# Kernel tuning notes

Hardware: AMD Instinct MI355X
Metric: run time of the kernel (lower is better)

## Reference

```python
import jax, jax.numpy as jnp
import numpy as np

N_LEVELS = 16; BASE = 16; SCALE = 2.0; L2HASH = 19; LEVEL_DIM = 2; BOUND = 2.0
RES = [int(np.ceil(BASE * SCALE ** i)) for i in range(N_LEVELS)]
# level-0 table size; the torch source uses embeddings[0].num_embeddings as the
# modulus for ALL levels (kept faithful). T0 = min(16^3, 2^19) = 4096.
T0 = min(RES[0] ** 3, 2 ** L2HASH)
# 4096 is a power of two, so hash % 4096 only depends on low 12 bits -> reduce
# primes mod T0 and work in int32 (matches torch's int64 math exactly).
PRIMES = (np.array([1, 2654435761, 805459861], dtype=np.int64) % T0).astype(np.int32)
# corner order matches the torch triple loop: dx outer, dy, dz inner
OFFS = np.array([[dx, dy, dz] for dx in (0, 1) for dy in (0, 1) for dz in (0, 1)], dtype=np.int32)


def _hash(c):
    # c: int32 [..., 3], already clamped to [0, res-1]
    return ((c[..., 0] * PRIMES[0]) ^ (c[..., 1] * PRIMES[1]) ^ (c[..., 2] * PRIMES[2])) % T0


def _hash_encode(pn, emb):
    # pn: [N,3] normalized positions; emb: [L, T0, 2]
    outs = []
    for li, res in enumerate(RES):
        scaled = (pn + 1.0) * 0.5 * (res - 1)            # [N,3]
        gc = jnp.floor(scaled).astype(jnp.int32)
        w = scaled - gc.astype(scaled.dtype)             # trilinear weights [N,3]
        corners = jnp.clip(gc[:, None, :] + OFFS[None], 0, res - 1)  # [N,8,3]
        f = emb[li][_hash(corners)]                      # gather -> [N,8,2]
        wx, wy, wz = w[:, 0:1], w[:, 1:2], w[:, 2:3]
        c00 = f[:, 0] * (1 - wx) + f[:, 1] * wx
        c01 = f[:, 2] * (1 - wx) + f[:, 3] * wx
        c10 = f[:, 4] * (1 - wx) + f[:, 5] * wx
        c11 = f[:, 6] * (1 - wx) + f[:, 7] * wx
        c0 = c00 * (1 - wy) + c01 * wy
        c1 = c10 * (1 - wy) + c11 * wy
        outs.append(c0 * (1 - wz) + c1 * wz)
    return jnp.concatenate(outs, -1)                     # [N, 32]


def _sh16(d):
    n = jnp.maximum(jnp.linalg.norm(d, axis=-1, keepdims=True), 1e-12)
    d = d / n
    x, y, z = d[..., 0], d[..., 1], d[..., 2]
    feats = [
        0.28209479177387814 * jnp.ones_like(x),
        -0.48860251190291987 * y, 0.48860251190291987 * z, -0.48860251190291987 * x,
        1.0925484305920792 * x * y, -1.0925484305920792 * y * z,
        0.31539156525252005 * (2 * z ** 2 - x ** 2 - y ** 2),
        -1.0925484305920792 * x * z, 0.5462742152960396 * (x ** 2 - y ** 2),
        -0.5900435899266435 * y * (3 * x ** 2 - y ** 2), 2.890611442640554 * x * y * z,
        -0.4570457994644658 * y * (4 * z ** 2 - x ** 2 - y ** 2),
        0.3731763325901154 * z * (2 * z ** 2 - 3 * x ** 2 - 3 * y ** 2),
        -0.4570457994644658 * x * (4 * z ** 2 - x ** 2 - y ** 2),
        1.445305721320277 * z * (x ** 2 - y ** 2),
        -0.5900435899266435 * x * (x ** 2 - 3 * y ** 2),
    ]
    return jnp.stack(feats, -1)                          # [N, 16]


def setup_inputs() -> dict:
    key = jax.random.key(0)
    ks = jax.random.split(key, 20)
    N = 1_000_000
    def lin(k, i, o):
        return jax.random.normal(k, (i, o), jnp.float32) * (1.0 / np.sqrt(i))
    return {
        'positions': jax.random.uniform(ks[0], (N, 3), jnp.float32),  # in [0,1) c [-bound,bound]
        'directions': jax.random.normal(ks[1], (N, 3), jnp.float32),
        'emb': jax.random.uniform(ks[2], (N_LEVELS, T0, LEVEL_DIM), jnp.float32, -1e-4, 1e-4),
        'gw0': lin(ks[3], 32, 64), 'gb0': jnp.zeros((64,), jnp.float32),
        'gw1': lin(ks[4], 64, 64), 'gb1': jnp.zeros((64,), jnp.float32),
        'dw': lin(ks[5], 64, 16), 'db': jnp.zeros((16,), jnp.float32),
        'cw0': lin(ks[6], 31, 64), 'cb0': jnp.zeros((64,), jnp.float32),
        'cw1': lin(ks[7], 64, 64), 'cb1': jnp.zeros((64,), jnp.float32),
        'cw2': lin(ks[8], 64, 64), 'cb2': jnp.zeros((64,), jnp.float32),
        'rw': lin(ks[9], 64, 3), 'rb': jnp.zeros((3,), jnp.float32),
    }


def reference(positions, directions, emb, gw0, gb0, gw1, gb1, dw, db,
              cw0, cb0, cw1, cb1, cw2, cb2, rw, rb):
    pn = positions / BOUND
    enc = _hash_encode(pn, emb)                          # [N,32]
    h = jax.nn.relu(enc @ gw0 + gb0)
    h = jax.nn.relu(h @ gw1 + gb1)
    g = h @ dw + db                                      # [N, 1+15]
    density = jnp.exp(g[:, 0:1] - 1.0)                   # exp activation, bias -1.0
    geo_feat = g[:, 1:]
    c = jnp.concatenate([geo_feat, _sh16(directions)], -1)  # [N,31]
    c = jax.nn.relu(c @ cw0 + cb0)
    c = c @ cw1 + cb1                                    # NOTE: no ReLU (faithful to source)
    c = c @ cw2 + cb2
    rgb = jax.nn.sigmoid(c @ rw + rb)
    return density, rgb
```

## Files before the change

kernel.cpp:

```cpp
#include <hip/hip_runtime.h>
#include <hip/hip_bf16.h>
#include <math.h>

#define BLK 256
#define TT  4096
#define WSETS 36

typedef short bf16x8 __attribute__((ext_vector_type(8)));
typedef float f32x4  __attribute__((ext_vector_type(4)));

__device__ __forceinline__ unsigned pk(float a, float b) {
  __hip_bfloat162 h = __float22bfloat162_rn(make_float2(a, b));
  unsigned r; __builtin_memcpy(&r, &h, sizeof(r));
  return r;
}
__device__ __forceinline__ bf16x8 mk8(unsigned w0, unsigned w1, unsigned w2, unsigned w3) {
  uint4 u; u.x = w0; u.y = w1; u.z = w2; u.w = w3;
  bf16x8 r; __builtin_memcpy(&r, &u, 16);
  return r;
}
__device__ __forceinline__ bf16x8 ld8(const uint4* __restrict__ wsW, int set, int lane) {
  uint4 u = wsW[set * 64 + lane];
  bf16x8 r; __builtin_memcpy(&r, &u, 16);
  return r;
}
__device__ __forceinline__ float bflo(unsigned w) {
  return __builtin_bit_cast(float, w << 16);
}
__device__ __forceinline__ float bfhi(unsigned w) {
  return __builtin_bit_cast(float, w & 0xFFFF0000u);
}
__device__ __forceinline__ f32x4 mfma16(bf16x8 a, bf16x8 b, f32x4 c) {
  return __builtin_amdgcn_mfma_f32_16x16x32_bf16(a, b, c, 0, 0, 0);
}

__global__ void ngp_pack(const float* __restrict__ emb,
                         const float* __restrict__ gw0, const float* __restrict__ gw1,
                         const float* __restrict__ dw,  const float* __restrict__ cw0,
                         const float* __restrict__ cw1, const float* __restrict__ cw2,
                         const float* __restrict__ rw,  unsigned* __restrict__ ws)
{
  int i = blockIdx.x * blockDim.x + threadIdx.x;
  if (i < 16 * TT) {
    const float* s = emb + 2 * (size_t)i;
    ws[i] = pk(s[0], s[1]);
    return;
  }
  i -= 16 * TT;
  if (i >= WSETS * 64) return;
  int s = i >> 6, l = i & 63;
  int q = l >> 4, p = l & 15;

  const float* W; int out = 64, mt = 0, kt = 0, typ = 0;
  if      (s < 4)  { W = gw0; mt = s; }
  else if (s < 12) { W = gw1; mt = (s - 4) >> 1;  kt = (s - 4) & 1; }
  else if (s < 14) { W = dw;  out = 16; kt = s - 12; }
  else if (s < 18) { W = cw0; mt = s - 14; typ = 1; }
  else if (s < 26) { W = cw1; mt = (s - 18) >> 1; kt = (s - 18) & 1; }
  else if (s < 34) { W = cw2; mt = (s - 26) >> 1; kt = (s - 26) & 1; }
  else             { W = rw;  out = 3; kt = s - 34; typ = 2; }
  int f = (out == 16) ? p : ((out == 3) ? p : mt * 16 + p);
  float v[8];
  #pragma unroll
  for (int j = 0; j < 8; ++j) {
    int k = kt * 32 + q * 8 + j;
    if (typ == 1)      v[j] = (k == 0) ? 0.0f : W[(k - 1) * 64 + f];
    else if (typ == 2) v[j] = (p < 3) ? W[k * 3 + p] : 0.0f;
    else               v[j] = W[k * out + f];
  }
  uint4 wv;
  wv.x = pk(v[0], v[1]); wv.y = pk(v[2], v[3]);
  wv.z = pk(v[4], v[5]); wv.w = pk(v[6], v[7]);
  ((uint4*)(ws + 16 * TT))[s * 64 + l] = wv;
}

__device__ __forceinline__ bf16x8 bfrag_pt(const unsigned (&ep)[16], int src, int q) {
  bf16x8 b;
  #pragma unroll
  for (int w = 0; w < 4; ++w) {
    int v0 = __shfl((int)ep[w],      src);
    int v1 = __shfl((int)ep[4 + w],  src);
    int v2 = __shfl((int)ep[8 + w],  src);
    int v3 = __shfl((int)ep[12 + w], src);
    int lo = (q & 1) ? v1 : v0;
    int hi = (q & 1) ? v3 : v2;
    unsigned word = (unsigned)((q & 2) ? hi : lo);
    b[2 * w]     = (short)(word & 0xFFFFu);
    b[2 * w + 1] = (short)(word >> 16);
  }
  return b;
}

template<int KT_>
__device__ __forceinline__ bf16x8 bfrag_u(const unsigned (&unt)[4][2], int q, int p) {
  bf16x8 b;
  #pragma unroll
  for (int w = 0; w < 4; ++w) {
    int src = (((2 * q + (w >> 1)) & 3) << 4) + p;
    int v0 = __shfl((int)unt[2 * KT_][w & 1],     src);
    int v1 = __shfl((int)unt[2 * KT_ + 1][w & 1], src);
    unsigned word = (unsigned)((q >> 1) ? v1 : v0);
    b[2 * w]     = (short)(word & 0xFFFFu);
    b[2 * w + 1] = (short)(word >> 16);
  }
  return b;
}

__device__ __forceinline__ bf16x8 bfrag_cat(const unsigned (&g2nt)[2], const unsigned (&shp)[8],
                                            int srcP, int q, int p) {
  bf16x8 b;
  #pragma unroll
  for (int w = 0; w < 4; ++w) {
    int srcG = (((2 * q + (w >> 1)) & 3) << 4) + p;
    int vg = __shfl((int)g2nt[w & 1], srcG);
    int v2 = __shfl((int)shp[w],      srcP);
    int v3 = __shfl((int)shp[4 + w],  srcP);
    unsigned word = (q < 2) ? (unsigned)vg : ((q == 2) ? (unsigned)v2 : (unsigned)v3);
    b[2 * w]     = (short)(word & 0xFFFFu);
    b[2 * w + 1] = (short)(word >> 16);
  }
  return b;
}

template<bool PRE, bool RELU>
__device__ __forceinline__ void layer64(const float* __restrict__ W, const uint4* __restrict__ wsW,
                                        int base, const float* __restrict__ bias,
                                        const unsigned (&uin)[4][4][2], unsigned (&uout)[4][4][2],
                                        int lane, int q, int p) {
  bf16x8 A[4][2];
  #pragma unroll
  for (int mt = 0; mt < 4; ++mt)
    #pragma unroll
    for (int kt = 0; kt < 2; ++kt) {
      if (PRE) {
        A[mt][kt] = ld8(wsW, base + mt * 2 + kt, lane);
      } else {
        const float* Wb = W + (kt * 32 + 8 * q) * 64 + mt * 16 + p;
        A[mt][kt] = mk8(pk(Wb[0 * 64], Wb[1 * 64]), pk(Wb[2 * 64], Wb[3 * 64]),
                        pk(Wb[4 * 64], Wb[5 * 64]), pk(Wb[6 * 64], Wb[7 * 64]));
      }
    }
  f32x4 bi[4];
  #pragma unroll
  for (int mt = 0; mt < 4; ++mt) bi[mt] = *(const f32x4*)(bias + mt * 16 + 4 * q);
  #pragma unroll
  for (int nt = 0; nt < 4; ++nt) {
    bf16x8 B0 = bfrag_u<0>(uin[nt], q, p);
    bf16x8 B1 = bfrag_u<1>(uin[nt], q, p);
    #pragma unroll
    for (int mt = 0; mt < 4; ++mt) {
      f32x4 acc = bi[mt];
      acc = mfma16(A[mt][0], B0, acc);
      acc = mfma16(A[mt][1], B1, acc);
      if (RELU) {
        acc.x = fmaxf(acc.x, 0.0f); acc.y = fmaxf(acc.y, 0.0f);
        acc.z = fmaxf(acc.z, 0.0f); acc.w = fmaxf(acc.w, 0.0f);
      }
      uout[nt][mt][0] = pk(acc.x, acc.y);
      uout[nt][mt][1] = pk(acc.z, acc.w);
    }
  }
}

template<bool PRE>
__global__ __launch_bounds__(BLK, 4)
void ngp_fused9(const float* __restrict__ pos,  const float* __restrict__ dirs,
                const float* __restrict__ emb,  const unsigned* __restrict__ wsTab,
                const float* __restrict__ gw0, const float* __restrict__ gb0,
                const float* __restrict__ gw1, const float* __restrict__ gb1,
                const float* __restrict__ dw,  const float* __restrict__ db,
                const float* __restrict__ cw0, const float* __restrict__ cb0,
                const float* __restrict__ cw1, const float* __restrict__ cb1,
                const float* __restrict__ cw2, const float* __restrict__ cb2,
                const float* __restrict__ rw,  const float* __restrict__ rb,
                float* __restrict__ outd, float* __restrict__ outrgb, int N)
{
  __shared__ unsigned tab[2][TT];

  const int tid  = threadIdx.x;
  const int lane = tid & 63, wave = tid >> 6;
  const int q = lane >> 4, p = lane & 15;
  const int idx = blockIdx.x * BLK + tid;
  const int ic = min(idx, N - 1);
  const int ptb = blockIdx.x * BLK + wave * 64;
  const uint4* wsW = (const uint4*)(wsTab + 16 * TT);

  const float pnx = pos[3 * ic + 0] * 0.5f;
  const float pny = pos[3 * ic + 1] * 0.5f;
  const float pnz = pos[3 * ic + 2] * 0.5f;

  auto stage = [&](int li) {
    if (PRE) {
      const uint4* s4 = (const uint4*)(wsTab + (size_t)li * TT);
      uint4* dst = (uint4*)tab[li & 1];
      #pragma unroll
      for (int j = 0; j < (TT / 4) / BLK; ++j)
        dst[tid + j * BLK] = s4[tid + j * BLK];
    } else {
      const f32x4* s4 = (const f32x4*)(emb + (size_t)li * (TT * 2));
      uint2* dst = (uint2*)tab[li & 1];
      #pragma unroll
      for (int j = 0; j < (TT / 2) / BLK; ++j) {
        f32x4 v = s4[tid + j * BLK];
        uint2 w; w.x = pk(v.x, v.y); w.y = pk(v.z, v.w);
        dst[tid + j * BLK] = w;
      }
    }
  };

  float enc[32];
  stage(0);
  __syncthreads();
  #pragma unroll
  for (int li = 0; li < 16; ++li) {
    if (li < 15) stage(li + 1);
    const unsigned* t = tab[li & 1];
    const int   res = 16 << li;
    const float rm1 = (float)(res - 1);
    float sx = (pnx + 1.0f) * 0.5f * rm1;
    float sy = (pny + 1.0f) * 0.5f * rm1;
    float sz = (pnz + 1.0f) * 0.5f * rm1;
    float fx = floorf(sx), fy = floorf(sy), fz = floorf(sz);
    float wx = sx - fx,    wy = sy - fy,    wz = sz - fz;
    int ix = (int)fx, iy = (int)fy, iz = (int)fz;
    int x0 = min(max(ix, 0),     res - 1), x1 = min(max(ix + 1, 0), res - 1);
    int y0 = min(max(iy, 0),     res - 1), y1 = min(max(iy + 1, 0), res - 1);
    int z0 = min(max(iz, 0),     res - 1), z1 = min(max(iz + 1, 0), res - 1);
    unsigned a0 = (unsigned)x0,         a1 = (unsigned)x1;
    unsigned b0 = (unsigned)y0 * 2481u, b1 = (unsigned)y1 * 2481u;
    unsigned d0 = (unsigned)z0 * 1941u, d1 = (unsigned)z1 * 1941u;
    unsigned w0 = t[(a0 ^ b0 ^ d0) & 4095u];
    unsigned w1 = t[(a0 ^ b0 ^ d1) & 4095u];
    unsigned w2 = t[(a0 ^ b1 ^ d0) & 4095u];
    unsigned w3 = t[(a0 ^ b1 ^ d1) & 4095u];
    unsigned w4 = t[(a1 ^ b0 ^ d0) & 4095u];
    unsigned w5 = t[(a1 ^ b0 ^ d1) & 4095u];
    unsigned w6 = t[(a1 ^ b1 ^ d0) & 4095u];
    unsigned w7 = t[(a1 ^ b1 ^ d1) & 4095u];
    float omx = 1.0f - wx, omy = 1.0f - wy, omz = 1.0f - wz;
    float c00x = bflo(w0) * omx + bflo(w1) * wx, c00y = bfhi(w0) * omx + bfhi(w1) * wx;
    float c01x = bflo(w2) * omx + bflo(w3) * wx, c01y = bfhi(w2) * omx + bfhi(w3) * wx;
    float c10x = bflo(w4) * omx + bflo(w5) * wx, c10y = bfhi(w4) * omx + bfhi(w5) * wx;
    float c11x = bflo(w6) * omx + bflo(w7) * wx, c11y = bfhi(w6) * omx + bfhi(w7) * wx;
    float e0x = c00x * omy + c01x * wy,  e0y = c00y * omy + c01y * wy;
    float e1x = c10x * omy + c11x * wy,  e1y = c10y * omy + c11y * wy;
    enc[2 * li + 0] = e0x * omz + e1x * wz;
    enc[2 * li + 1] = e0y * omz + e1y * wz;
    __syncthreads();
  }
  unsigned encp[16];
  #pragma unroll
  for (int m = 0; m < 16; ++m) encp[m] = pk(enc[2 * m], enc[2 * m + 1]);

  unsigned shp[8];
  {
    float ddx = dirs[3 * ic + 0], ddy = dirs[3 * ic + 1], ddz = dirs[3 * ic + 2];
    float nrm = fmaxf(sqrtf(ddx * ddx + ddy * ddy + ddz * ddz), 1e-12f);
    float x = ddx / nrm, y = ddy / nrm, z = ddz / nrm;
    float xx = x * x, yy = y * y, zz = z * z;
    float xy = x * y, yz = y * z, xz = x * z;
    float sh0  = 0.28209479177387814f;
    float sh1  = -0.48860251190291987f * y;
    float sh2  =  0.48860251190291987f * z;
    float sh3  = -0.48860251190291987f * x;
    float sh4  =  1.0925484305920792f * xy;
    float sh5  = -1.0925484305920792f * yz;
    float sh6  =  0.31539156525252005f * (2.0f * zz - xx - yy);
    float sh7  = -1.0925484305920792f * xz;
    float sh8  =  0.5462742152960396f * (xx - yy);
    float sh9  = -0.5900435899266435f * y * (3.0f * xx - yy);
    float sh10 =  2.890611442640554f * xy * z;
    float sh11 = -0.4570457994644658f * y * (4.0f * zz - xx - yy);
    float sh12 =  0.3731763325901154f * z * (2.0f * zz - 3.0f * xx - 3.0f * yy);
    float sh13 = -0.4570457994644658f * x * (4.0f * zz - xx - yy);
    float sh14 =  1.445305721320277f * z * (xx - yy);
    float sh15 = -0.5900435899266435f * x * (xx - 3.0f * yy);
    shp[0] = pk(sh0,  sh1);  shp[1] = pk(sh2,  sh3);
    shp[2] = pk(sh4,  sh5);  shp[3] = pk(sh6,  sh7);
    shp[4] = pk(sh8,  sh9);  shp[5] = pk(sh10, sh11);
    shp[6] = pk(sh12, sh13); shp[7] = pk(sh14, sh15);
  }

  unsigned uA[4][4][2], uB[4][4][2];

  {
    bf16x8 A[4];
    #pragma unroll
    for (int mt = 0; mt < 4; ++mt) {
      if (PRE) {
        A[mt] = ld8(wsW, mt, lane);
      } else {
        const float* Wb = gw0 + (8 * q) * 64 + mt * 16 + p;
        A[mt] = mk8(pk(Wb[0 * 64], Wb[1 * 64]), pk(Wb[2 * 64], Wb[3 * 64]),
                    pk(Wb[4 * 64], Wb[5 * 64]), pk(Wb[6 * 64], Wb[7 * 64]));
      }
    }
    f32x4 bi[4];
    #pragma unroll
    for (int mt = 0; mt < 4; ++mt) bi[mt] = *(const f32x4*)(gb0 + mt * 16 + 4 * q);
    #pragma unroll
    for (int nt = 0; nt < 4; ++nt) {
      bf16x8 B = bfrag_pt(encp, nt * 16 + p, q);
      #pragma unroll
      for (int mt = 0; mt < 4; ++mt) {
        f32x4 acc = mfma16(A[mt], B, bi[mt]);
        acc.x = fmaxf(acc.x, 0.0f); acc.y = fmaxf(acc.y, 0.0f);
        acc.z = fmaxf(acc.z, 0.0f); acc.w = fmaxf(acc.w, 0.0f);
        uA[nt][mt][0] = pk(acc.x, acc.y);
        uA[nt][mt][1] = pk(acc.z, acc.w);
      }
    }
  }

  layer64<PRE, true>(gw1, wsW, 4, gb1, uA, uB, lane, q, p);

  unsigned g2[4][2];
  {
    bf16x8 A[2];
    #pragma unroll
    for (int kt = 0; kt < 2; ++kt) {
      if (PRE) {
        A[kt] = ld8(wsW, 12 + kt, lane);
      } else {
        const float* Wb = dw + (kt * 32 + 8 * q) * 16 + p;
        A[kt] = mk8(pk(Wb[0 * 16], Wb[1 * 16]), pk(Wb[2 * 16], Wb[3 * 16]),
                    pk(Wb[4 * 16], Wb[5 * 16]), pk(Wb[6 * 16], Wb[7 * 16]));
      }
    }
    f32x4 bi = *(const f32x4*)(db + 4 * q);
    #pragma unroll
    for (int nt = 0; nt < 4; ++nt) {
      bf16x8 B0 = bfrag_u<0>(uB[nt], q, p);
      bf16x8 B1 = bfrag_u<1>(uB[nt], q, p);
      f32x4 acc = mfma16(A[0], B0, bi);
      acc = mfma16(A[1], B1, acc);
      if (q == 0) {
        int pt = ptb + nt * 16 + p;
        if (pt < N) outd[pt] = expf(acc.x - 1.0f);
      }
      g2[nt][0] = pk(acc.x, acc.y);
      g2[nt][1] = pk(acc.z, acc.w);
    }
  }

  {
    bf16x8 A[4];
    #pragma unroll
    for (int mt = 0; mt < 4; ++mt) {
      if (PRE) {
        A[mt] = ld8(wsW, 14 + mt, lane);
      } else {
        float v[8];
        #pragma unroll
        for (int j = 0; j < 8; ++j) {
          int k = 8 * q + j;
          v[j] = (k == 0) ? 0.0f : cw0[(k - 1) * 64 + mt * 16 + p];
        }
        A[mt] = mk8(pk(v[0], v[1]), pk(v[2], v[3]), pk(v[4], v[5]), pk(v[6], v[7]));
      }
    }
    f32x4 bi[4];
    #pragma unroll
    for (int mt = 0; mt < 4; ++mt) bi[mt] = *(const f32x4*)(cb0 + mt * 16 + 4 * q);
    #pragma unroll
    for (int nt = 0; nt < 4; ++nt) {
      bf16x8 B = bfrag_cat(g2[nt], shp, nt * 16 + p, q, p);
      #pragma unroll
      for (int mt = 0; mt < 4; ++mt) {
        f32x4 acc = mfma16(A[mt], B, bi[mt]);
        acc.x = fmaxf(acc.x, 0.0f); acc.y = fmaxf(acc.y, 0.0f);
        acc.z = fmaxf(acc.z, 0.0f); acc.w = fmaxf(acc.w, 0.0f);
        uA[nt][mt][0] = pk(acc.x, acc.y);
        uA[nt][mt][1] = pk(acc.z, acc.w);
      }
    }
  }

  layer64<PRE, false>(cw1, wsW, 18, cb1, uA, uB, lane, q, p);
  layer64<PRE, false>(cw2, wsW, 26, cb2, uB, uA, lane, q, p);

  {
    bf16x8 A[2];
    #pragma unroll
    for (int kt = 0; kt < 2; ++kt) {
      if (PRE) {
        A[kt] = ld8(wsW, 34 + kt, lane);
      } else {
        float v[8];
        #pragma unroll
        for (int j = 0; j < 8; ++j) {
          int k = kt * 32 + 8 * q + j;
          v[j] = (p < 3) ? rw[k * 3 + p] : 0.0f;
        }
        A[kt] = mk8(pk(v[0], v[1]), pk(v[2], v[3]), pk(v[4], v[5]), pk(v[6], v[7]));
      }
    }
    float r0 = rb[0], r1 = rb[1], r2 = rb[2];
    #pragma unroll
    for (int nt = 0; nt < 4; ++nt) {
      bf16x8 B0 = bfrag_u<0>(uA[nt], q, p);
      bf16x8 B1 = bfrag_u<1>(uA[nt], q, p);
      f32x4 acc;
      acc.x = (q == 0) ? r0 : 0.0f;
      acc.y = (q == 0) ? r1 : 0.0f;
      acc.z = (q == 0) ? r2 : 0.0f;
      acc.w = 0.0f;
      acc = mfma16(A[0], B0, acc);
      acc = mfma16(A[1], B1, acc);
      if (q == 0) {
        int pt = ptb + nt * 16 + p;
        if (pt < N) {
          outrgb[3 * pt + 0] = 1.0f / (1.0f + expf(-acc.x));
          outrgb[3 * pt + 1] = 1.0f / (1.0f + expf(-acc.y));
          outrgb[3 * pt + 2] = 1.0f / (1.0f + expf(-acc.z));
        }
      }
    }
  }
}

extern "C" void kernel_launch(void* const* d_in, const int* in_sizes, int n_in,
                              void* d_out, int out_size, void* d_ws, size_t ws_size,
                              hipStream_t stream) {
  const float* pos  = (const float*)d_in[0];
  const float* dirs = (const float*)d_in[1];
  const float* emb  = (const float*)d_in[2];
  const float* gw0  = (const float*)d_in[3];
  const float* gb0  = (const float*)d_in[4];
  const float* gw1  = (const float*)d_in[5];
  const float* gb1  = (const float*)d_in[6];
  const float* dw   = (const float*)d_in[7];
  const float* db   = (const float*)d_in[8];
  const float* cw0  = (const float*)d_in[9];
  const float* cb0  = (const float*)d_in[10];
  const float* cw1  = (const float*)d_in[11];
  const float* cb1  = (const float*)d_in[12];
  const float* cw2  = (const float*)d_in[13];
  const float* cb2  = (const float*)d_in[14];
  const float* rw   = (const float*)d_in[15];
  const float* rb   = (const float*)d_in[16];

  const int N = in_sizes[0] / 3;
  float* outd   = (float*)d_out;
  float* outrgb = outd + N;

  const size_t need = (size_t)(16 * TT) * 4 + (size_t)(WSETS * 64) * 16;
  const bool pre = (ws_size >= need);
  unsigned* wsTab = (unsigned*)d_ws;

  const int grid = (N + BLK - 1) / BLK;
  if (pre) {
    const int packN = 16 * TT + WSETS * 64;
    hipLaunchKernelGGL(ngp_pack, dim3((packN + 255) / 256), dim3(256), 0, stream,
                       emb, gw0, gw1, dw, cw0, cw1, cw2, rw, wsTab);
    hipLaunchKernelGGL((ngp_fused9<true>), dim3(grid), dim3(BLK), 0, stream,
                       pos, dirs, emb, wsTab, gw0, gb0, gw1, gb1, dw, db,
                       cw0, cb0, cw1, cb1, cw2, cb2, rw, rb, outd, outrgb, N);
  } else {
    hipLaunchKernelGGL((ngp_fused9<false>), dim3(grid), dim3(BLK), 0, stream,
                       pos, dirs, emb, wsTab, gw0, gb0, gw1, gb1, dw, db,
                       cw0, cb0, cw1, cb1, cw2, cb2, rw, rb, outd, outrgb, N);
  }
}
```

Before: 162.4 us.

## Process two points per thread to amortize per-level hash table staging

Each block now handles 512 points with 256 threads. Every thread encodes two points against each staged level table, then runs the MLP twice. This halves the number of blocks and so halves the global-to-LDS table staging and barrier cost per point. In exchange, registers per thread go up because there are two encoding arrays, which may hurt occupancy under the launch bounds, and there are fewer blocks to spread across the GPU.

```diff
diff --git a/kernel.cpp b/kernel.cpp
--- a/kernel.cpp
+++ b/kernel.cpp
@@ -3,6 +3,7 @@
 #include <math.h>
 
 #define BLK 256
+#define PTS (2 * BLK)
 #define TT  4096
 #define WSETS 36
 
@@ -164,7 +165,7 @@
 
 template<bool PRE>
 __global__ __launch_bounds__(BLK, 4)
-void ngp_fused9(const float* __restrict__ pos,  const float* __restrict__ dirs,
+void ngp_fusedA(const float* __restrict__ pos,  const float* __restrict__ dirs,
                 const float* __restrict__ emb,  const unsigned* __restrict__ wsTab,
                 const float* __restrict__ gw0, const float* __restrict__ gb0,
                 const float* __restrict__ gw1, const float* __restrict__ gb1,
@@ -180,14 +181,18 @@
   const int tid  = threadIdx.x;
   const int lane = tid & 63, wave = tid >> 6;
   const int q = lane >> 4, p = lane & 15;
-  const int idx = blockIdx.x * BLK + tid;
-  const int ic = min(idx, N - 1);
-  const int ptb = blockIdx.x * BLK + wave * 64;
+  const int base = blockIdx.x * PTS;
+  const int idx0 = base + tid, idx1 = idx0 + BLK;
+  const int ic0 = min(idx0, N - 1), ic1 = min(idx1, N - 1);
+  const int ptb0 = base + wave * 64, ptb1 = ptb0 + BLK;
   const uint4* wsW = (const uint4*)(wsTab + 16 * TT);
 
-  const float pnx = pos[3 * ic + 0] * 0.5f;
-  const float pny = pos[3 * ic + 1] * 0.5f;
-  const float pnz = pos[3 * ic + 2] * 0.5f;
+  const float p0x = pos[3 * ic0 + 0] * 0.5f;
+  const float p0y = pos[3 * ic0 + 1] * 0.5f;
+  const float p0z = pos[3 * ic0 + 2] * 0.5f;
+  const float p1x = pos[3 * ic1 + 0] * 0.5f;
+  const float p1y = pos[3 * ic1 + 1] * 0.5f;
+  const float p1z = pos[3 * ic1 + 2] * 0.5f;
 
   auto stage = [&](int li) {
     if (PRE) {
@@ -208,18 +213,11 @@
     }
   };
 
-  float enc[32];
-  stage(0);
-  __syncthreads();
-  #pragma unroll
-  for (int li = 0; li < 16; ++li) {
-    if (li < 15) stage(li + 1);
-    const unsigned* t = tab[li & 1];
-    const int   res = 16 << li;
-    const float rm1 = (float)(res - 1);
-    float sx = (pnx + 1.0f) * 0.5f * rm1;
-    float sy = (pny + 1.0f) * 0.5f * rm1;
-    float sz = (pnz + 1.0f) * 0.5f * rm1;
+  auto encL = [&](const unsigned* t, int res, float rm1,
+                  float px, float py, float pz) -> unsigned {
+    float sx = (px + 1.0f) * 0.5f * rm1;
+    float sy = (py + 1.0f) * 0.5f * rm1;
+    float sz = (pz + 1.0f) * 0.5f * rm1;
     float fx = floorf(sx), fy = floorf(sy), fz = floorf(sz);
     float wx = sx - fx,    wy = sy - fy,    wz = sz - fz;
     int ix = (int)fx, iy = (int)fy, iz = (int)fz;
@@ -244,179 +242,193 @@
     float c11x = bflo(w6) * omx + bflo(w7) * wx, c11y = bfhi(w6) * omx + bfhi(w7) * wx;
     float e0x = c00x * omy + c01x * wy,  e0y = c00y * omy + c01y * wy;
     float e1x = c10x * omy + c11x * wy,  e1y = c10y * omy + c11y * wy;
-    enc[2 * li + 0] = e0x * omz + e1x * wz;
-    enc[2 * li + 1] = e0y * omz + e1y * wz;
+    return pk(e0x * omz + e1x * wz, e0y * omz + e1y * wz);
+  };
+
+  unsigned encp0[16], encp1[16];
+  stage(0);
+  __syncthreads();
+  #pragma unroll
+  for (int li = 0; li < 16; ++li) {
+    if (li < 15) stage(li + 1);
+    const unsigned* t = tab[li & 1];
+    const int   res = 16 << li;
+    const float rm1 = (float)(res - 1);
+    encp0[li] = encL(t, res, rm1, p0x, p0y, p0z);
+    encp1[li] = encL(t, res, rm1, p1x, p1y, p1z);
     __syncthreads();
   }
-  unsigned encp[16];
-  #pragma unroll
-  for (int m = 0; m < 16; ++m) encp[m] = pk(enc[2 * m], enc[2 * m + 1]);
-
-  unsigned shp[8];
-  {
-    float ddx = dirs[3 * ic + 0], ddy = dirs[3 * ic + 1], ddz = dirs[3 * ic + 2];
-    float nrm = fmaxf(sqrtf(ddx * ddx + ddy * ddy + ddz * ddz), 1e-12f);
-    float x = ddx / nrm, y = ddy / nrm, z = ddz / nrm;
-    float xx = x * x, yy = y * y, zz = z * z;
-    float xy = x * y, yz = y * z, xz = x * z;
-    float sh0  = 0.28209479177387814f;
-    float sh1  = -0.48860251190291987f * y;
-    float sh2  =  0.48860251190291987f * z;
-    float sh3  = -0.48860251190291987f * x;
-    float sh4  =  1.0925484305920792f * xy;
-    float sh5  = -1.0925484305920792f * yz;
-    float sh6  =  0.31539156525252005f * (2.0f * zz - xx - yy);
-    float sh7  = -1.0925484305920792f * xz;
-    float sh8  =  0.5462742152960396f * (xx - yy);
-    float sh9  = -0.5900435899266435f * y * (3.0f * xx - yy);
-    float sh10 =  2.890611442640554f * xy * z;
-    float sh11 = -0.4570457994644658f * y * (4.0f * zz - xx - yy);
-    float sh12 =  0.3731763325901154f * z * (2.0f * zz - 3.0f * xx - 3.0f * yy);
-    float sh13 = -0.4570457994644658f * x * (4.0f * zz - xx - yy);
-    float sh14 =  1.445305721320277f * z * (xx - yy);
-    float sh15 = -0.5900435899266435f * x * (xx - 3.0f * yy);
-    shp[0] = pk(sh0,  sh1);  shp[1] = pk(sh2,  sh3);
-    shp[2] = pk(sh4,  sh5);  shp[3] = pk(sh6,  sh7);
-    shp[4] = pk(sh8,  sh9);  shp[5] = pk(sh10, sh11);
-    shp[6] = pk(sh12, sh13); shp[7] = pk(sh14, sh15);
-  }
-
-  unsigned uA[4][4][2], uB[4][4][2];
-
-  {
-    bf16x8 A[4];
-    #pragma unroll
-    for (int mt = 0; mt < 4; ++mt) {
-      if (PRE) {
-        A[mt] = ld8(wsW, mt, lane);
-      } else {
-        const float* Wb = gw0 + (8 * q) * 64 + mt * 16 + p;
-        A[mt] = mk8(pk(Wb[0 * 64], Wb[1 * 64]), pk(Wb[2 * 64], Wb[3 * 64]),
-                    pk(Wb[4 * 64], Wb[5 * 64]), pk(Wb[6 * 64], Wb[7 * 64]));
-      }
-    }
-    f32x4 bi[4];
-    #pragma unroll
-    for (int mt = 0; mt < 4; ++mt) bi[mt] = *(const f32x4*)(gb0 + mt * 16 + 4 * q);
-    #pragma unroll
-    for (int nt = 0; nt < 4; ++nt) {
-      bf16x8 B = bfrag_pt(encp, nt * 16 + p, q);
+
+  auto mlp = [&](const unsigned (&encp)[16], int ic, int ptb) {
+    unsigned shp[8];
+    {
+      float ddx = dirs[3 * ic + 0], ddy = dirs[3 * ic + 1], ddz = dirs[3 * ic + 2];
+      float nrm = fmaxf(sqrtf(ddx * ddx + ddy * ddy + ddz * ddz), 1e-12f);
+      float x = ddx / nrm, y = ddy / nrm, z = ddz / nrm;
+      float xx = x * x, yy = y * y, zz = z * z;
+      float xy = x * y, yz = y * z, xz = x * z;
+      float sh0  = 0.28209479177387814f;
+      float sh1  = -0.48860251190291987f * y;
+      float sh2  =  0.48860251190291987f * z;
+      float sh3  = -0.48860251190291987f * x;
+      float sh4  =  1.0925484305920792f * xy;
+      float sh5  = -1.0925484305920792f * yz;
+      float sh6  =  0.31539156525252005f * (2.0f * zz - xx - yy);
+      float sh7  = -1.0925484305920792f * xz;
+      float sh8  =  0.5462742152960396f * (xx - yy);
+      float sh9  = -0.5900435899266435f * y * (3.0f * xx - yy);
+      float sh10 =  2.890611442640554f * xy * z;
+      float sh11 = -0.4570457994644658f * y * (4.0f * zz - xx - yy);
+      float sh12 =  0.3731763325901154f * z * (2.0f * zz - 3.0f * xx - 3.0f * yy);
+      float sh13 = -0.4570457994644658f * x * (4.0f * zz - xx - yy);
+      float sh14 =  1.445305721320277f * z * (xx - yy);
+      float sh15 = -0.5900435899266435f * x * (xx - 3.0f * yy);
+      shp[0] = pk(sh0,  sh1);  shp[1] = pk(sh2,  sh3);
+      shp[2] = pk(sh4,  sh5);  shp[3] = pk(sh6,  sh7);
+      shp[4] = pk(sh8,  sh9);  shp[5] = pk(sh10, sh11);
+      shp[6] = pk(sh12, sh13); shp[7] = pk(sh14, sh15);
+    }
+
+    unsigned uA[4][4][2], uB[4][4][2];
+
+    {
+      bf16x8 A[4];
       #pragma unroll
       for (int mt = 0; mt < 4; ++mt) {
-        f32x4 acc = mfma16(A[mt], B, bi[mt]);
-        acc.x = fmaxf(acc.x, 0.0f); acc.y = fmaxf(acc.y, 0.0f);
-        acc.z = fmaxf(acc.z, 0.0f); acc.w = fmaxf(acc.w, 0.0f);
-        uA[nt][mt][0] = pk(acc.x, acc.y);
-        uA[nt][mt][1] = pk(acc.z, acc.w);
-      }
-    }
-  }
-
-  layer64<PRE, true>(gw1, wsW, 4, gb1, uA, uB, lane, q, p);
-
-  unsigned g2[4][2];
-  {
-    bf16x8 A[2];
-    #pragma unroll
-    for (int kt = 0; kt < 2; ++kt) {
-      if (PRE) {
-        A[kt] = ld8(wsW, 12 + kt, lane);
-      } else {
-        const float* Wb = dw + (kt * 32 + 8 * q) * 16 + p;
-        A[kt] = mk8(pk(Wb[0 * 16], Wb[1 * 16]), pk(Wb[2 * 16], Wb[3 * 16]),
-                    pk(Wb[4 * 16], Wb[5 * 16]), pk(Wb[6 * 16], Wb[7 * 16]));
-      }
-    }
-    f32x4 bi = *(const f32x4*)(db + 4 * q);
-    #pragma unroll
-    for (int nt = 0; nt < 4; ++nt) {
-      bf16x8 B0 = bfrag_u<0>(uB[nt], q, p);
-      bf16x8 B1 = bfrag_u<1>(uB[nt], q, p);
-      f32x4 acc = mfma16(A[0], B0, bi);
-      acc = mfma16(A[1], B1, acc);
-      if (q == 0) {
-        int pt = ptb + nt * 16 + p;
-        if (pt < N) outd[pt] = expf(acc.x - 1.0f);
-      }
-      g2[nt][0] = pk(acc.x, acc.y);
-      g2[nt][1] = pk(acc.z, acc.w);
-    }
-  }
-
-  {
-    bf16x8 A[4];
-    #pragma unroll
-    for (int mt = 0; mt < 4; ++mt) {
-      if (PRE) {
-        A[mt] = ld8(wsW, 14 + mt, lane);
-      } else {
-        float v[8];
+        if (PRE) {
+          A[mt] = ld8(wsW, mt, lane);
+        } else {
+          const float* Wb = gw0 + (8 * q) * 64 + mt * 16 + p;
+          A[mt] = mk8(pk(Wb[0 * 64], Wb[1 * 64]), pk(Wb[2 * 64], Wb[3 * 64]),
+                      pk(Wb[4 * 64], Wb[5 * 64]), pk(Wb[6 * 64], Wb[7 * 64]));
+        }
+      }
+      f32x4 bi[4];
+      #pragma unroll
+      for (int mt = 0; mt < 4; ++mt) bi[mt] = *(const f32x4*)(gb0 + mt * 16 + 4 * q);
+      #pragma unroll
+      for (int nt = 0; nt < 4; ++nt) {
+        bf16x8 B = bfrag_pt(encp, nt * 16 + p, q);
         #pragma unroll
-        for (int j = 0; j < 8; ++j) {
-          int k = 8 * q + j;
-          v[j] = (k == 0) ? 0.0f : cw0[(k - 1) * 64 + mt * 16 + p];
-        }
-        A[mt] = mk8(pk(v[0], v[1]), pk(v[2], v[3]), pk(v[4], v[5]), pk(v[6], v[7]));
-      }
-    }
-    f32x4 bi[4];
-    #pragma unroll
-    for (int mt = 0; mt < 4; ++mt) bi[mt] = *(const f32x4*)(cb0 + mt * 16 + 4 * q);
-    #pragma unroll
-    for (int nt = 0; nt < 4; ++nt) {
-      bf16x8 B = bfrag_cat(g2[nt], shp, nt * 16 + p, q, p);
+        for (int mt = 0; mt < 4; ++mt) {
+          f32x4 acc = mfma16(A[mt], B, bi[mt]);
+          acc.x = fmaxf(acc.x, 0.0f); acc.y = fmaxf(acc.y, 0.0f);
+          acc.z = fmaxf(acc.z, 0.0f); acc.w = fmaxf(acc.w, 0.0f);
+          uA[nt][mt][0] = pk(acc.x, acc.y);
+          uA[nt][mt][1] = pk(acc.z, acc.w);
+        }
+      }
+    }
+
+    layer64<PRE, true>(gw1, wsW, 4, gb1, uA, uB, lane, q, p);
+
+    unsigned g2[4][2];
+    {
+      bf16x8 A[2];
+      #pragma unroll
+      for (int kt = 0; kt < 2; ++kt) {
+        if (PRE) {
+          A[kt] = ld8(wsW, 12 + kt, lane);
+        } else {
+          const float* Wb = dw + (kt * 32 + 8 * q) * 16 + p;
+          A[kt] = mk8(pk(Wb[0 * 16], Wb[1 * 16]), pk(Wb[2 * 16], Wb[3 * 16]),
+                      pk(Wb[4 * 16], Wb[5 * 16]), pk(Wb[6 * 16], Wb[7 * 16]));
+        }
+      }
+      f32x4 bi = *(const f32x4*)(db + 4 * q);
+      #pragma unroll
+      for (int nt = 0; nt < 4; ++nt) {
+        bf16x8 B0 = bfrag_u<0>(uB[nt], q, p);
+        bf16x8 B1 = bfrag_u<1>(uB[nt], q, p);
+        f32x4 acc = mfma16(A[0], B0, bi);
+        acc = mfma16(A[1], B1, acc);
+        if (q == 0) {
+          int pt = ptb + nt * 16 + p;
+          if (pt < N) outd[pt] = expf(acc.x - 1.0f);
+        }
+        g2[nt][0] = pk(acc.x, acc.y);
+        g2[nt][1] = pk(acc.z, acc.w);
+      }
+    }
+
+    {
+      bf16x8 A[4];
       #pragma unroll
       for (int mt = 0; mt < 4; ++mt) {
-        f32x4 acc = mfma16(A[mt], B, bi[mt]);
-        acc.x = fmaxf(acc.x, 0.0f); acc.y = fmaxf(acc.y, 0.0f);
-        acc.z = fmaxf(acc.z, 0.0f); acc.w = fmaxf(acc.w, 0.0f);
-        uA[nt][mt][0] = pk(acc.x, acc.y);
-        uA[nt][mt][1] = pk(acc.z, acc.w);
-      }
-    }
-  }
-
-  layer64<PRE, false>(cw1, wsW, 18, cb1, uA, uB, lane, q, p);
-  layer64<PRE, false>(cw2, wsW, 26, cb2, uB, uA, lane, q, p);
-
-  {
-    bf16x8 A[2];
-    #pragma unroll
-    for (int kt = 0; kt < 2; ++kt) {
-      if (PRE) {
-        A[kt] = ld8(wsW, 34 + kt, lane);
-      } else {
-        float v[8];
+        if (PRE) {
+          A[mt] = ld8(wsW, 14 + mt, lane);
+        } else {
+          float v[8];
+          #pragma unroll
+          for (int j = 0; j < 8; ++j) {
+            int k = 8 * q + j;
+            v[j] = (k == 0) ? 0.0f : cw0[(k - 1) * 64 + mt * 16 + p];
+          }
+          A[mt] = mk8(pk(v[0], v[1]), pk(v[2], v[3]), pk(v[4], v[5]), pk(v[6], v[7]));
+        }
+      }
+      f32x4 bi[4];
+      #pragma unroll
+      for (int mt = 0; mt < 4; ++mt) bi[mt] = *(const f32x4*)(cb0 + mt * 16 + 4 * q);
+      #pragma unroll
+      for (int nt = 0; nt < 4; ++nt) {
+        bf16x8 B = bfrag_cat(g2[nt], shp, nt * 16 + p, q, p);
         #pragma unroll
-        for (int j = 0; j < 8; ++j) {
-          int k = kt * 32 + 8 * q + j;
-          v[j] = (p < 3) ? rw[k * 3 + p] : 0.0f;
-        }
-        A[kt] = mk8(pk(v[0], v[1]), pk(v[2], v[3]), pk(v[4], v[5]), pk(v[6], v[7]));
-      }
-    }
-    float r0 = rb[0], r1 = rb[1], r2 = rb[2];
-    #pragma unroll
-    for (int nt = 0; nt < 4; ++nt) {
-      bf16x8 B0 = bfrag_u<0>(uA[nt], q, p);
-      bf16x8 B1 = bfrag_u<1>(uA[nt], q, p);
-      f32x4 acc;
-      acc.x = (q == 0) ? r0 : 0.0f;
-      acc.y = (q == 0) ? r1 : 0.0f;
-      acc.z = (q == 0) ? r2 : 0.0f;
-      acc.w = 0.0f;
-      acc = mfma16(A[0], B0, acc);
-      acc = mfma16(A[1], B1, acc);
-      if (q == 0) {
-        int pt = ptb + nt * 16 + p;
-        if (pt < N) {
-          outrgb[3 * pt + 0] = 1.0f / (1.0f + expf(-acc.x));
-          outrgb[3 * pt + 1] = 1.0f / (1.0f + expf(-acc.y));
-          outrgb[3 * pt + 2] = 1.0f / (1.0f + expf(-acc.z));
-        }
-      }
-    }
-  }
+        for (int mt = 0; mt < 4; ++mt) {
+          f32x4 acc = mfma16(A[mt], B, bi[mt]);
+          acc.x = fmaxf(acc.x, 0.0f); acc.y = fmaxf(acc.y, 0.0f);
+          acc.z = fmaxf(acc.z, 0.0f); acc.w = fmaxf(acc.w, 0.0f);
+          uA[nt][mt][0] = pk(acc.x, acc.y);
+          uA[nt][mt][1] = pk(acc.z, acc.w);
+        }
+      }
+    }
+
+    layer64<PRE, false>(cw1, wsW, 18, cb1, uA, uB, lane, q, p);
+    layer64<PRE, false>(cw2, wsW, 26, cb2, uB, uA, lane, q, p);
+
+    {
+      bf16x8 A[2];
+      #pragma unroll
+      for (int kt = 0; kt < 2; ++kt) {
+        if (PRE) {
+          A[kt] = ld8(wsW, 34 + kt, lane);
+        } else {
+          float v[8];
+          #pragma unroll
+          for (int j = 0; j < 8; ++j) {
+            int k = kt * 32 + 8 * q + j;
+            v[j] = (p < 3) ? rw[k * 3 + p] : 0.0f;
+          }
+          A[kt] = mk8(pk(v[0], v[1]), pk(v[2], v[3]), pk(v[4], v[5]), pk(v[6], v[7]));
+        }
+      }
+      float r0 = rb[0], r1 = rb[1], r2 = rb[2];
+      #pragma unroll
+      for (int nt = 0; nt < 4; ++nt) {
+        bf16x8 B0 = bfrag_u<0>(uA[nt], q, p);
+        bf16x8 B1 = bfrag_u<1>(uA[nt], q, p);
+        f32x4 acc;
+        acc.x = (q == 0) ? r0 : 0.0f;
+        acc.y = (q == 0) ? r1 : 0.0f;
+        acc.z = (q == 0) ? r2 : 0.0f;
+        acc.w = 0.0f;
+        acc = mfma16(A[0], B0, acc);
+        acc = mfma16(A[1], B1, acc);
+        if (q == 0) {
+          int pt = ptb + nt * 16 + p;
+          if (pt < N) {
+            outrgb[3 * pt + 0] = 1.0f / (1.0f + expf(-acc.x));
+            outrgb[3 * pt + 1] = 1.0f / (1.0f + expf(-acc.y));
+            outrgb[3 * pt + 2] = 1.0f / (1.0f + expf(-acc.z));
+          }
+        }
+      }
+    }
+  };
+
+  mlp(encp0, ic0, ptb0);
+  mlp(encp1, ic1, ptb1);
 }
 
 extern "C" void kernel_launch(void* const* d_in, const int* in_sizes, int n_in,
@@ -448,16 +460,16 @@
   const bool pre = (ws_size >= need);
   unsigned* wsTab = (unsigned*)d_ws;
 
-  const int grid = (N + BLK - 1) / BLK;
+  const int grid = (N + PTS - 1) / PTS;
   if (pre) {
     const int packN = 16 * TT + WSETS * 64;
     hipLaunchKernelGGL(ngp_pack, dim3((packN + 255) / 256), dim3(256), 0, stream,
                        emb, gw0, gw1, dw, cw0, cw1, cw2, rw, wsTab);
-    hipLaunchKernelGGL((ngp_fused9<true>), dim3(grid), dim3(BLK), 0, stream,
+    hipLaunchKernelGGL((ngp_fusedA<true>), dim3(grid), dim3(BLK), 0, stream,
                        pos, dirs, emb, wsTab, gw0, gb0, gw1, gb1, dw, db,
                        cw0, cb0, cw1, cb1, cw2, cb2, rw, rb, outd, outrgb, N);
   } else {
-    hipLaunchKernelGGL((ngp_fused9<false>), dim3(grid), dim3(BLK), 0, stream,
+    hipLaunchKernelGGL((ngp_fusedA<false>), dim3(grid), dim3(BLK), 0, stream,
                        pos, dirs, emb, wsTab, gw0, gb0, gw1, gb1, dw, db,
                        cw0, cb0, cw1, cb1, cw2, cb2, rw, rb, outd, outrgb, N);
   }
```

Measured after the change: 303.9 us. +87.1%, slower.
